# Performance work log

Hardware: AMD Instinct MI355X
Metric: run time of the kernel (lower is better)

## Reference

```python
import jax, jax.numpy as jnp
import numpy as np

N, C_IN, C_OUT, T, V = 64, 128, 128, 128, 25
REL = C_IN // 8  # rel_channels = 16


def setup_inputs() -> dict:
    key = jax.random.key(0)
    ks = jax.random.split(key, 12)
    s_in = 1.0 / np.sqrt(C_IN)
    s_rel = 1.0 / np.sqrt(REL)
    return {
        "x": jax.random.normal(ks[0], (N, C_IN, T, V), jnp.float32),
        "A": jax.random.normal(ks[1], (V, V), jnp.float32),
        "alpha": jnp.float32(1.0),
        "W1": jax.random.normal(ks[2], (REL, C_IN), jnp.float32) * s_in,
        "b1": jnp.zeros((REL,), jnp.float32),
        "W2": jax.random.normal(ks[3], (REL, C_IN), jnp.float32) * s_in,
        "b2": jnp.zeros((REL,), jnp.float32),
        "W3": jax.random.normal(ks[4], (C_OUT, C_IN), jnp.float32) * s_in,
        "b3": jnp.zeros((C_OUT,), jnp.float32),
        "W4": jax.random.normal(ks[5], (C_OUT, REL), jnp.float32) * s_rel,
        "b4": jnp.zeros((C_OUT,), jnp.float32),
    }


def reference(x, A, alpha, W1, b1, W2, b2, W3, b3, W4, b4):
    # conv1(x).mean(-2) and conv2(x).mean(-2): 1x1 conv is linear, so mean over
    # T commutes with it -> compute mean first to avoid an (N,REL,T,V) temp.
    xm = x.mean(axis=2)                                        # (N, C, V)
    x1 = jnp.einsum('rc,ncv->nrv', W1, xm) + b1[None, :, None]  # (N, R, V)
    x2 = jnp.einsum('rc,ncv->nrv', W2, xm) + b2[None, :, None]  # (N, R, V)
    x3 = jnp.einsum('oc,nctv->notv', W3, x) + b3[None, :, None, None]  # (N,O,T,V)
    # tanh of broadcasted pairwise difference: (N, R, V, V)
    d = jnp.tanh(x1[:, :, :, None] - x2[:, :, None, :])
    # conv4 (1x1 over channel dim) -> learned per-channel adjacency
    adj = jnp.einsum('or,nrvu->novu', W4, d) + b4[None, :, None, None]
    adj = adj * alpha + A[None, None, :, :]                    # (N, O, V, V)
    return jnp.einsum('ncvu,nctv->nctu', adj, x3)              # (N, O, T, V)
```

## Files before the change

### kernel.cpp

```cpp
#include <hip/hip_runtime.h>


#define NB   64
#define CIN  128
#define COUT 128
#define TT   128
#define VV   25
#define REL  16

#define JT 25
#define KT 4
#define XF_BYTES (JT * KT * 1024)
#define XH_BYTES 51200
#define X3_STRIDE 1040
#define LDS_BYTES (64 * X3_STRIDE)
#define TSTRIDE 416
#define XMP_PLANE (NB * CIN * VV)

typedef __attribute__((ext_vector_type(8))) short bf16x8;
typedef __attribute__((ext_vector_type(4))) float f32x4;

__device__ inline short f2bf(float f) {
    unsigned u = __float_as_uint(f);
    u += 0x7fff + ((u >> 16) & 1);
    return (short)(u >> 16);
}

__launch_bounds__(256)
__global__ void k_prep(const float* __restrict__ x, float* __restrict__ xmp,
                       char* __restrict__ Xf) {
    __shared__ float tile[32 * TSTRIDE];
    int tid = threadIdx.x;
    int kt = blockIdx.x >> 3, tb = blockIdx.x & 7, n = blockIdx.y;
    int c0 = kt * 32;

    const float* src = x + (size_t)(n * CIN + c0) * 3200 + tb * 400;
#pragma unroll
    for (int p = 0; p < 13; ++p) {
        int i = tid + p * 256;
        if (i < 3200) {
            int c = i / 100, q = i - c * 100;
            int sw = ((c >> 3) & 1) << 4;
            *reinterpret_cast<float4*>(&tile[c * TSTRIDE + ((q * 4) ^ sw)]) =
                *reinterpret_cast<const float4*>(src + (size_t)c * 3200 + q * 4);
        }
    }
    __syncthreads();

#pragma unroll
    for (int pp = 0; pp < 4; ++pp) {
        int p = tid + pp * 256;
        if (p < 800) {
            int c = p / 25, v = p - c * 25;
            int sw = ((c >> 3) & 1) << 4;
            float s = 0.f;
#pragma unroll
            for (int t = 0; t < 16; ++t) s += tile[c * TSTRIDE + ((t * 25 + v) ^ sw)];
            xmp[(size_t)tb * XMP_PLANE + ((size_t)n * CIN + c0 + c) * VV + v] = s;
        }
    }

    char* dst = Xf + (size_t)(n * 8 + tb) * XF_BYTES + (size_t)kt * 25600;
    for (int ch = tid; ch < 1600; ch += 256) {
        int l = ch & 63, jt = ch >> 6;
        int j = jt * 16 + (l & 15);
        int cl = 8 * (l >> 4);
        int sw = ((l >> 4) & 1) << 4;
        bf16x8 v;
#pragma unroll
        for (int b = 0; b < 8; ++b)
            v[b] = f2bf(tile[(cl + b) * TSTRIDE + (j ^ sw)]);
        *reinterpret_cast<bf16x8*>(dst + (size_t)ch * 16) = v;
    }
}

__global__ void k_adj(const float* __restrict__ xmp,
                      const float* __restrict__ A, const float* __restrict__ alphap,
                      const float* __restrict__ W1, const float* __restrict__ b1,
                      const float* __restrict__ W2, const float* __restrict__ b2,
                      const float* __restrict__ W4, const float* __restrict__ b4,
                      const float* __restrict__ W3, char* __restrict__ W3f,
                      char* __restrict__ adjT) {
    __shared__ char adjS[32 * 2048];
    __shared__ float xms[CIN * VV];
    __shared__ float W1s[REL * CIN];
    __shared__ float W2s[REL * CIN];
    __shared__ float x1s[REL * VV];
    __shared__ float x2s[REL * VV];
    __shared__ float W4s[32 * REL];
    __shared__ float b4s[32];

    int tid = threadIdx.x;
    int n = blockIdx.x;
    int o0 = blockIdx.y * 32;

    if (n == 0) {
#pragma unroll
        for (int pass = 0; pass < 2; ++pass) {
            int chunk = blockIdx.y * 512 + pass * 256 + tid;
            int l = chunk & 63;
            int frag = chunk >> 6;
            int ct = frag >> 2, kt = frag & 3;
            int c = ct * 16 + (l & 15);
            int kb = kt * 32 + 8 * (l >> 4);
            const float4 f0 = *reinterpret_cast<const float4*>(&W3[(size_t)c * CIN + kb]);
            const float4 f1 = *reinterpret_cast<const float4*>(&W3[(size_t)c * CIN + kb + 4]);
            bf16x8 vv;
            vv[0] = f2bf(f0.x); vv[1] = f2bf(f0.y); vv[2] = f2bf(f0.z); vv[3] = f2bf(f0.w);
            vv[4] = f2bf(f1.x); vv[5] = f2bf(f1.y); vv[6] = f2bf(f1.z); vv[7] = f2bf(f1.w);
            *reinterpret_cast<bf16x8*>(W3f + (size_t)chunk * 16) = vv;
        }
    }

    for (int i = tid; i < 16384; i += 256) reinterpret_cast<float*>(adjS)[i] = 0.f;
    for (int i = tid; i < CIN * VV; i += 256) {
        float s = 0.f;
#pragma unroll
        for (int tb = 0; tb < 8; ++tb)
            s += xmp[(size_t)tb * XMP_PLANE + (size_t)n * CIN * VV + i];
        xms[i] = s * (1.0f / TT);
    }
    for (int i = tid; i < REL * CIN; i += 256) { W1s[i] = W1[i]; W2s[i] = W2[i]; }
    for (int i = tid; i < 32 * REL; i += 256) W4s[i] = W4[o0 * REL + i];
    if (tid < 32) b4s[tid] = b4[o0 + tid];
    __syncthreads();

    for (int task = tid; task < 2 * REL * VV; task += 256) {
        int rv = task % (REL * VV);
        int which = task / (REL * VV);
        int r = rv / VV, v = rv % VV;
        const float* Ws = which ? W2s : W1s;
        float s = 0.f;
#pragma unroll 8
        for (int c = 0; c < CIN; ++c) s = fmaf(Ws[r * CIN + c], xms[c * VV + v], s);
        s += which ? b2[r] : b1[r];
        (which ? x2s : x1s)[rv] = s;
    }
    __syncthreads();

    float alpha = alphap[0];
    for (int p = tid; p < VV * VV; p += 256) {
        int v = p / VV, u = p % VV;
        float d[REL];
#pragma unroll
        for (int r = 0; r < REL; ++r) d[r] = tanhf(x1s[r * VV + v] - x2s[r * VV + u]);
        float Avu = A[v * VV + u];
        int off = (u >> 4) * 1024 + (((u & 15) + 16 * (v >> 3)) * 16) + (v & 7) * 2;
        for (int oo = 0; oo < 32; ++oo) {
            float s = 0.f;
#pragma unroll
            for (int r = 0; r < REL; ++r) s = fmaf(W4s[oo * REL + r], d[r], s);
            float val = alpha * (s + b4s[oo]) + Avu;
            *(short*)(adjS + oo * 2048 + off) = f2bf(val);
        }
    }
    __syncthreads();

    float4* dst = reinterpret_cast<float4*>(adjT + (size_t)(n * COUT + o0) * 2048);
    const float4* src = reinterpret_cast<const float4*>(adjS);
    for (int i = tid; i < 4096; i += 256) dst[i] = src[i];
}

__launch_bounds__(1024)
__global__ void k_main(const char* __restrict__ Xf, const char* __restrict__ W3f,
                       const float* __restrict__ b3, const char* __restrict__ adjT,
                       float* __restrict__ out) {
    __shared__ __align__(16) char lds[LDS_BYTES];

    int tid = threadIdx.x;
    int tb = blockIdx.x, n = blockIdx.y;
    int lane = tid & 63, w = tid >> 6;
    int g = lane >> 4, lr = lane & 15;
    int ct = w >> 1, jh = w & 1;
    int jt0 = jh ? 13 : 0;
    int njt = jh ? 12 : 13;

    const char* xfb = Xf + (size_t)(n * 8 + tb) * XF_BYTES;

    f32x4 acc[13];
#pragma unroll
    for (int u = 0; u < 13; ++u) acc[u] = f32x4{0.f, 0.f, 0.f, 0.f};

#pragma unroll
    for (int h = 0; h < 2; ++h) {
#pragma unroll
        for (int q = 0; q < 4; ++q) {
            int chunk = tid + q * 1024;
            if (chunk < 3200)
                *reinterpret_cast<bf16x8*>(lds + (size_t)chunk * 16) =
                    *reinterpret_cast<const bf16x8*>(
                        xfb + (size_t)h * XH_BYTES + (size_t)chunk * 16);
        }
        __syncthreads();
#pragma unroll
        for (int kk = 0; kk < 2; ++kk) {
            int kt = h * 2 + kk;
            bf16x8 a = *reinterpret_cast<const bf16x8*>(
                W3f + (size_t)((ct * 4 + kt) * 64 + lane) * 16);
#pragma unroll
            for (int u = 0; u < 13; ++u) {
                if (u < njt) {
                    int jt = jt0 + u;
                    bf16x8 bx = *reinterpret_cast<const bf16x8*>(
                        lds + (size_t)((kk * JT + jt) * 64 + lane) * 16);
                    acc[u] = __builtin_amdgcn_mfma_f32_16x16x32_bf16(a, bx, acc[u], 0, 0, 0);
                }
            }
        }
        __syncthreads();
    }

    float bv[4];
#pragma unroll
    for (int r = 0; r < 4; ++r) bv[r] = b3[ct * 16 + 4 * g + r];

    const char* adjTb = adjT + (size_t)(n * COUT) * 2048;
    int t0 = tb * 16;

#pragma unroll
    for (int hh = 0; hh < 2; ++hh) {
        if ((ct >> 2) == hh) {
            int cb = (ct & 3) * 16 + 4 * g;
#pragma unroll
            for (int u = 0; u < 13; ++u) {
                if (u < njt) {
                    int j = (jt0 + u) * 16 + lr;
                    int t = j / 25, v = j - t * 25;
                    int off = (t + 16 * (v >> 3)) * 16 + (v & 7) * 2;
#pragma unroll
                    for (int r = 0; r < 4; ++r)
                        *(short*)(lds + (size_t)(cb + r) * X3_STRIDE + off) =
                            f2bf(acc[u][r] + bv[r]);
                }
            }
        }
#pragma unroll
        for (int z = 0; z < 7; ++z) {
            int idx = tid + z * 1024;
            if (idx < 7168) {
                int c = idx / 112;
                int rem = idx - c * 112;
                int t = rem / 7, qq = rem - t * 7;
                *(short*)(lds + (size_t)c * X3_STRIDE + (t + 48) * 16 + 2 + qq * 2) = 0;
            }
        }
        __syncthreads();

#pragma unroll
        for (int i = 0; i < 4; ++i) {
            int cl = w * 4 + i;
            int c = hh * 64 + cl;
            bf16x8 a = *reinterpret_cast<const bf16x8*>(
                lds + (size_t)cl * X3_STRIDE + lane * 16);
            const bf16x8* bp = reinterpret_cast<const bf16x8*>(adjTb + (size_t)c * 2048);
            bf16x8 b0 = bp[lane];
            bf16x8 b1 = bp[64 + lane];
            f32x4 z = {0.f, 0.f, 0.f, 0.f};
            f32x4 d0 = __builtin_amdgcn_mfma_f32_16x16x32_bf16(a, b0, z, 0, 0, 0);
            f32x4 d1 = __builtin_amdgcn_mfma_f32_16x16x32_bf16(a, b1, z, 0, 0, 0);
            float* ob = out + ((size_t)(n * COUT + c) * TT + t0) * VV;
#pragma unroll
            for (int rr = 0; rr < 4; ++rr) {
                int t = 4 * g + rr;
                ob[(size_t)t * VV + lr] = d0[rr];
                if (lr < 9) ob[(size_t)t * VV + 16 + lr] = d1[rr];
            }
        }
        __syncthreads();
    }
}

extern "C" void kernel_launch(void* const* d_in, const int* in_sizes, int n_in,
                              void* d_out, int out_size, void* d_ws, size_t ws_size,
                              hipStream_t stream) {
    const float* x     = (const float*)d_in[0];
    const float* A     = (const float*)d_in[1];
    const float* alpha = (const float*)d_in[2];
    const float* W1    = (const float*)d_in[3];
    const float* b1    = (const float*)d_in[4];
    const float* W2    = (const float*)d_in[5];
    const float* b2    = (const float*)d_in[6];
    const float* W3    = (const float*)d_in[7];
    const float* b3    = (const float*)d_in[8];
    const float* W4    = (const float*)d_in[9];
    const float* b4    = (const float*)d_in[10];
    float* out = (float*)d_out;

    float* xmp = (float*)d_ws;
    char* adjT = (char*)d_ws + 6553600;
    char* W3f  = (char*)d_ws + 6553600 + 16777216;
    char* Xf   = (char*)d_ws + 6553600 + 16777216 + 32768;

    k_prep<<<dim3(32, NB), 256, 0, stream>>>(x, xmp, Xf);
    k_adj<<<dim3(NB, 4), 256, 0, stream>>>(xmp, A, alpha, W1, b1, W2, b2, W4, b4,
                                           W3, W3f, adjT);
    k_main<<<dim3(TT / 16, NB), 1024, 0, stream>>>(Xf, W3f, b3, adjT, out);
}
```

Baseline: 126.4 us.

## Stream both X halves via async global-to-LDS loads and overlap with MFMA

The main kernel now issues direct global-to-LDS loads for both K halves of the X tile up front, into an LDS buffer enlarged to hold both. It then uses partial vmcnt waits so the first half's MFMAs can start while the second half is still loading. The pad-zeroing is hoisted out of the per-half loop, and some __syncthreads are replaced by raw s_barrier with manual waitcnts. The bf16 packing in the prep and adj kernels now uses the v_cvt_pk_bf16_f32 instruction. The larger LDS footprint and the hand-written wait counts add occupancy and correctness risk.

```diff
diff --git a/kernel.cpp b/kernel.cpp
--- a/kernel.cpp
+++ b/kernel.cpp
@@ -13,7 +13,7 @@
 #define XF_BYTES (JT * KT * 1024)
 #define XH_BYTES 51200
 #define X3_STRIDE 1040
-#define LDS_BYTES (64 * X3_STRIDE)
+#define LDS_BYTES 102400
 #define TSTRIDE 416
 #define XMP_PLANE (NB * CIN * VV)
 
@@ -24,6 +24,12 @@
     unsigned u = __float_as_uint(f);
     u += 0x7fff + ((u >> 16) & 1);
     return (short)(u >> 16);
+}
+
+__device__ inline unsigned cvtpk(float lo, float hi) {
+    unsigned r;
+    asm("v_cvt_pk_bf16_f32 %0, %1, %2" : "=v"(r) : "v"(lo), "v"(hi));
+    return r;
 }
 
 __launch_bounds__(256)
@@ -66,11 +72,13 @@
         int j = jt * 16 + (l & 15);
         int cl = 8 * (l >> 4);
         int sw = ((l >> 4) & 1) << 4;
-        bf16x8 v;
-#pragma unroll
-        for (int b = 0; b < 8; ++b)
-            v[b] = f2bf(tile[(cl + b) * TSTRIDE + (j ^ sw)]);
-        *reinterpret_cast<bf16x8*>(dst + (size_t)ch * 16) = v;
+        float f[8];
+#pragma unroll
+        for (int b = 0; b < 8; ++b) f[b] = tile[(cl + b) * TSTRIDE + (j ^ sw)];
+        uint4 vv;
+        vv.x = cvtpk(f[0], f[1]); vv.y = cvtpk(f[2], f[3]);
+        vv.z = cvtpk(f[4], f[5]); vv.w = cvtpk(f[6], f[7]);
+        *reinterpret_cast<uint4*>(dst + (size_t)ch * 16) = vv;
     }
 }
 
@@ -105,10 +113,10 @@
             int kb = kt * 32 + 8 * (l >> 4);
             const float4 f0 = *reinterpret_cast<const float4*>(&W3[(size_t)c * CIN + kb]);
             const float4 f1 = *reinterpret_cast<const float4*>(&W3[(size_t)c * CIN + kb + 4]);
-            bf16x8 vv;
-            vv[0] = f2bf(f0.x); vv[1] = f2bf(f0.y); vv[2] = f2bf(f0.z); vv[3] = f2bf(f0.w);
-            vv[4] = f2bf(f1.x); vv[5] = f2bf(f1.y); vv[6] = f2bf(f1.z); vv[7] = f2bf(f1.w);
-            *reinterpret_cast<bf16x8*>(W3f + (size_t)chunk * 16) = vv;
+            uint4 vv;
+            vv.x = cvtpk(f0.x, f0.y); vv.y = cvtpk(f0.z, f0.w);
+            vv.z = cvtpk(f1.x, f1.y); vv.w = cvtpk(f1.z, f1.w);
+            *reinterpret_cast<uint4*>(W3f + (size_t)chunk * 16) = vv;
         }
     }
 
@@ -177,37 +185,71 @@
 
     const char* xfb = Xf + (size_t)(n * 8 + tb) * XF_BYTES;
 
-    f32x4 acc[13];
-#pragma unroll
-    for (int u = 0; u < 13; ++u) acc[u] = f32x4{0.f, 0.f, 0.f, 0.f};
-
 #pragma unroll
     for (int h = 0; h < 2; ++h) {
 #pragma unroll
         for (int q = 0; q < 4; ++q) {
             int chunk = tid + q * 1024;
             if (chunk < 3200)
-                *reinterpret_cast<bf16x8*>(lds + (size_t)chunk * 16) =
-                    *reinterpret_cast<const bf16x8*>(
-                        xfb + (size_t)h * XH_BYTES + (size_t)chunk * 16);
-        }
-        __syncthreads();
-#pragma unroll
-        for (int kk = 0; kk < 2; ++kk) {
-            int kt = h * 2 + kk;
-            bf16x8 a = *reinterpret_cast<const bf16x8*>(
-                W3f + (size_t)((ct * 4 + kt) * 64 + lane) * 16);
-#pragma unroll
-            for (int u = 0; u < 13; ++u) {
-                if (u < njt) {
-                    int jt = jt0 + u;
-                    bf16x8 bx = *reinterpret_cast<const bf16x8*>(
-                        lds + (size_t)((kk * JT + jt) * 64 + lane) * 16);
-                    acc[u] = __builtin_amdgcn_mfma_f32_16x16x32_bf16(a, bx, acc[u], 0, 0, 0);
-                }
+                __builtin_amdgcn_global_load_lds(
+                    (const __attribute__((address_space(1))) void*)
+                        (xfb + (size_t)h * XH_BYTES + (size_t)chunk * 16),
+                    (__attribute__((address_space(3))) void*)
+                        (lds + (size_t)h * XH_BYTES + (size_t)chunk * 16),
+                    16, 0, 0);
+        }
+    }
+
+    f32x4 acc[13];
+#pragma unroll
+    for (int u = 0; u < 13; ++u) acc[u] = f32x4{0.f, 0.f, 0.f, 0.f};
+
+    if (w < 2) { asm volatile("s_waitcnt vmcnt(4)" ::: "memory"); }
+    else       { asm volatile("s_waitcnt vmcnt(3)" ::: "memory"); }
+    __builtin_amdgcn_s_barrier();
+
+#pragma unroll
+    for (int kk = 0; kk < 2; ++kk) {
+        bf16x8 a = *reinterpret_cast<const bf16x8*>(
+            W3f + (size_t)((ct * 4 + kk) * 64 + lane) * 16);
+#pragma unroll
+        for (int u = 0; u < 13; ++u) {
+            if (u < njt) {
+                int jt = jt0 + u;
+                bf16x8 bx = *reinterpret_cast<const bf16x8*>(
+                    lds + (size_t)((kk * JT + jt) * 64 + lane) * 16);
+                acc[u] = __builtin_amdgcn_mfma_f32_16x16x32_bf16(a, bx, acc[u], 0, 0, 0);
             }
         }
-        __syncthreads();
+    }
+
+    asm volatile("s_waitcnt vmcnt(0)" ::: "memory");
+    __builtin_amdgcn_s_barrier();
+#pragma unroll
+    for (int kk = 0; kk < 2; ++kk) {
+        bf16x8 a = *reinterpret_cast<const bf16x8*>(
+            W3f + (size_t)((ct * 4 + 2 + kk) * 64 + lane) * 16);
+#pragma unroll
+        for (int u = 0; u < 13; ++u) {
+            if (u < njt) {
+                int jt = jt0 + u;
+                bf16x8 bx = *reinterpret_cast<const bf16x8*>(
+                    lds + XH_BYTES + (size_t)((kk * JT + jt) * 64 + lane) * 16);
+                acc[u] = __builtin_amdgcn_mfma_f32_16x16x32_bf16(a, bx, acc[u], 0, 0, 0);
+            }
+        }
+    }
+    __builtin_amdgcn_s_barrier();
+
+#pragma unroll
+    for (int z = 0; z < 7; ++z) {
+        int idx = tid + z * 1024;
+        if (idx < 7168) {
+            int c = idx / 112;
+            int rem = idx - c * 112;
+            int t = rem / 7, qq = rem - t * 7;
+            *(short*)(lds + (size_t)c * X3_STRIDE + (t + 48) * 16 + 2 + qq * 2) = 0;
+        }
     }
 
     float bv[4];
@@ -234,17 +276,8 @@
                 }
             }
         }
-#pragma unroll
-        for (int z = 0; z < 7; ++z) {
-            int idx = tid + z * 1024;
-            if (idx < 7168) {
-                int c = idx / 112;
-                int rem = idx - c * 112;
-                int t = rem / 7, qq = rem - t * 7;
-                *(short*)(lds + (size_t)c * X3_STRIDE + (t + 48) * 16 + 2 + qq * 2) = 0;
-            }
-        }
-        __syncthreads();
+        asm volatile("s_waitcnt lgkmcnt(0)" ::: "memory");
+        __builtin_amdgcn_s_barrier();
 
 #pragma unroll
         for (int i = 0; i < 4; ++i) {
@@ -266,7 +299,7 @@
                 if (lr < 9) ob[(size_t)t * VV + 16 + lr] = d1[rr];
             }
         }
-        __syncthreads();
+        __builtin_amdgcn_s_barrier();
     }
 }
 
```

New measurement: 125.9 us. No clear change (-0.4%).
